# Kernel optimization log

Measured on AMD Instinct MI355X. Metric: run time of the kernel, lower is better.

## Reference

```python
import jax, jax.numpy as jnp
import numpy as np
import math

DIM = 1024
THETA = 10000.0


def rope_cos_sin(seq_len, dim, dtype=jnp.float32):
    # freqs over pairs: 1/theta^(2i/dim), angles = t * freq
    inv = 1.0 / (THETA ** (jnp.arange(0, dim, 2, dtype=jnp.float32) / dim))  # [dim/2]
    t = jnp.arange(seq_len, dtype=jnp.float32)
    ang = jnp.outer(t, inv)  # [S, dim/2]
    return jnp.cos(ang).astype(dtype), jnp.sin(ang).astype(dtype)


def apply_rotary(x, cos, sin):
    # x: [B, S, D]; treat consecutive pairs as complex (xr + i*xi)
    B, S, D = x.shape
    xr = x[..., 0::2]  # [B, S, D/2]
    xi = x[..., 1::2]
    or_ = xr * cos - xi * sin
    oi_ = xr * sin + xi * cos
    # interleave back: (..., D/2, 2) -> (..., D)
    return jnp.stack([or_, oi_], axis=-1).reshape(B, S, D)


def setup_inputs() -> dict:
    key = jax.random.key(0)
    ks = jax.random.split(key, 5)
    B, S, D = 4, 2048, DIM
    x = jax.random.normal(ks[0], (B, S, D), dtype=jnp.float32)
    s = 1.0 / math.sqrt(D)
    wq = jax.random.normal(ks[1], (D, D), dtype=jnp.float32) * s
    wk = jax.random.normal(ks[2], (D, D), dtype=jnp.float32) * s
    wv = jax.random.normal(ks[3], (D, D), dtype=jnp.float32) * s
    wo = jax.random.normal(ks[4], (D, D), dtype=jnp.float32) * s
    return {"x": x, "wq": wq, "wk": wk, "wv": wv, "wo": wo}


def reference(x, wq, wk, wv, wo):
    B, S, D = x.shape
    xq = jnp.einsum('bsd,ed->bse', x, wq)  # Linear: x @ W^T
    xk = jnp.einsum('bsd,ed->bse', x, wk)
    xv = jnp.einsum('bsd,ed->bse', x, wv)
    cos, sin = rope_cos_sin(S, D, x.dtype)
    xq = apply_rotary(xq, cos, sin)
    xk = apply_rotary(xk, cos, sin)
    scores = jnp.einsum('bqd,bkd->bqk', xq, xk) / jnp.sqrt(jnp.asarray(D, x.dtype))
    attn = jax.nn.softmax(scores, axis=-1)  # no causal mask in original
    out = jnp.einsum('bqk,bkd->bqd', attn, xv)
    return jnp.einsum('bsd,ed->bse', out, wo)
```

## Files before the change

kernel.cpp:

```cpp
#include <hip/hip_runtime.h>
#include <math.h>

typedef __attribute__((ext_vector_type(8))) short short8;
typedef __attribute__((ext_vector_type(4))) float f32x4;
typedef unsigned short u16;

__device__ __forceinline__ float b2f(u16 u) {
    union { unsigned u; float f; } c; c.u = ((unsigned)u) << 16; return c.f;
}
__device__ __forceinline__ u16 f2b(float f) {
    unsigned u = __float_as_uint(f);
    u += 0x7fffu + ((u >> 16) & 1u);
    return (u16)(u >> 16);
}

__device__ __forceinline__ void gl_lds16(const u16* g, u16* l) {
    __builtin_amdgcn_global_load_lds(
        (const __attribute__((address_space(1))) void*)g,
        (__attribute__((address_space(3))) void*)l,
        16, 0, 0);
}

__device__ __forceinline__ void wgbar() {
    asm volatile("" ::: "memory");
    __builtin_amdgcn_s_barrier();
    asm volatile("" ::: "memory");
}

__global__ __launch_bounds__(256) void cvt_f32_bf16(const float* __restrict__ src,
                                                    u16* __restrict__ dst, int n) {
    const int i = (blockIdx.x * 256 + threadIdx.x) * 8;
    if (i >= n) return;
    const float4 a = *(const float4*)&src[i];
    const float4 b = *(const float4*)&src[i + 4];
    short8 o;
    o[0] = (short)f2b(a.x); o[1] = (short)f2b(a.y);
    o[2] = (short)f2b(a.z); o[3] = (short)f2b(a.w);
    o[4] = (short)f2b(b.x); o[5] = (short)f2b(b.y);
    o[6] = (short)f2b(b.z); o[7] = (short)f2b(b.w);
    *(short8*)&dst[i] = o;
}

__global__ __launch_bounds__(256) void cvt_weights(
    const float* __restrict__ w0, const float* __restrict__ w1,
    const float* __restrict__ w2, const float* __restrict__ w3,
    u16* __restrict__ dst) {
    const int z = blockIdx.z;
    const float* src = (z == 0) ? w0 : (z == 1) ? w1 : (z == 2) ? w2 : w3;
    const int i = (blockIdx.x * 256 + threadIdx.x) * 8;
    const float4 a = *(const float4*)&src[i];
    const float4 b = *(const float4*)&src[i + 4];
    short8 o;
    o[0] = (short)f2b(a.x); o[1] = (short)f2b(a.y);
    o[2] = (short)f2b(a.z); o[3] = (short)f2b(a.w);
    o[4] = (short)f2b(b.x); o[5] = (short)f2b(b.y);
    o[6] = (short)f2b(b.z); o[7] = (short)f2b(b.w);
    *(short8*)&dst[(long)z * 1024 * 1024 + i] = o;
}

template<typename OT>
__device__ __forceinline__ void gemm256_body(
    const u16* __restrict__ A, const u16* __restrict__ W, OT* __restrict__ C,
    int lda, int ldw, int ldc, int K, float scale)
{
    __shared__ u16 lsA[2][2][8192];
    __shared__ u16 lsB[2][2][8192];

    const int m0 = blockIdx.y * 256;
    const int n0 = blockIdx.x * 256;
    const int t = threadIdx.x;
    const int lane = t & 63;
    const int w = t >> 6;
    const int wm = (w & 1) * 128;
    const int wn = (w >> 1) * 64;
    const int fr = lane & 15;
    const int fq = lane >> 4;

    const int srow = t >> 2;
    const int scol = (t & 3) * 8;
    const u16* pA0 = A + (long)(m0 + srow) * lda + scol;
    const u16* pA1 = A + (long)(m0 + 128 + srow) * lda + scol;
    const u16* pW0 = W + (long)(n0 + srow) * ldw + scol;
    const u16* pW1 = W + (long)(n0 + 128 + srow) * ldw + scol;
    const int tld = t * 8;

    f32x4 acc[8][4];
#pragma unroll
    for (int i = 0; i < 8; ++i)
#pragma unroll
        for (int j = 0; j < 4; ++j)
            acc[i][j] = (f32x4){0.f, 0.f, 0.f, 0.f};

    const int aoff = (wm + fr) * 32 + fq * 8;
    const int boff = (wn + fr) * 32 + fq * 8;

#define STAGE256(buf, h, ko) do { \
    gl_lds16(pA0 + (ko), &lsA[buf][h][tld]); \
    gl_lds16(pA1 + (ko), &lsA[buf][h][4096 + tld]); \
    gl_lds16(pW0 + (ko), &lsB[buf][h][tld]); \
    gl_lds16(pW1 + (ko), &lsB[buf][h][4096 + tld]); \
} while (0)

    const int nt = K >> 6;
    STAGE256(0, 0, 0);
    STAGE256(0, 1, 32);
    asm volatile("s_waitcnt vmcnt(4)" ::: "memory");
    wgbar();

    for (int tt = 0; tt < nt; ++tt) {
        const int p = tt & 1;
        const int kn = (tt + 1) << 6;
#pragma unroll
        for (int h = 0; h < 2; ++h) {
            short8 af[8], bfr[4];
#pragma unroll
            for (int m = 0; m < 8; ++m)
                af[m] = *(const short8*)&lsA[p][h][aoff + m * 512];
#pragma unroll
            for (int n = 0; n < 4; ++n)
                bfr[n] = *(const short8*)&lsB[p][h][boff + n * 512];
            if (tt + 1 < nt) {
                STAGE256(p ^ 1, h, kn + h * 32);
                asm volatile("s_waitcnt vmcnt(4)" ::: "memory");
            } else {
                asm volatile("s_waitcnt vmcnt(0)" ::: "memory");
            }
            wgbar();
            __builtin_amdgcn_s_setprio(1);
#pragma unroll
            for (int m = 0; m < 8; ++m)
#pragma unroll
                for (int n = 0; n < 4; ++n)
                    acc[m][n] = __builtin_amdgcn_mfma_f32_16x16x32_bf16(
                        af[m], bfr[n], acc[m][n], 0, 0, 0);
            __builtin_amdgcn_s_setprio(0);
        }
    }
#undef STAGE256

#pragma unroll
    for (int m = 0; m < 8; ++m) {
        const int row0 = m0 + wm + m * 16 + fq * 4;
#pragma unroll
        for (int n = 0; n < 4; ++n) {
            const int col = n0 + wn + n * 16 + fr;
#pragma unroll
            for (int r = 0; r < 4; ++r) {
                const float val = acc[m][n][r] * scale;
                if (sizeof(OT) == 2) {
                    ((u16*)C)[(long)(row0 + r) * ldc + col] = f2b(val);
                } else {
                    ((float*)C)[(long)(row0 + r) * ldc + col] = val;
                }
            }
        }
    }
}

template<typename OT>
__global__ __launch_bounds__(512, 2) void gemm256_bt(
    const u16* __restrict__ A, const u16* __restrict__ W, OT* __restrict__ C,
    int lda, int ldw, int ldc, int K,
    long sA, long sW, long sC, float scale)
{
    const int z = blockIdx.z;
    gemm256_body<OT>(A + (long)z * sA, W + (long)z * sW, C + (long)z * sC,
                     lda, ldw, ldc, K, scale);
}

__global__ __launch_bounds__(512, 2) void gemm256_dual(
    const u16* __restrict__ A0, const u16* __restrict__ W0, u16* __restrict__ C0,
    int lda0, int ldw0, int ldc0, long sA0, long sW0, long sC0, float scale0,
    const u16* __restrict__ A1, const u16* __restrict__ W1, u16* __restrict__ C1,
    int lda1, int ldw1, int ldc1, long sA1, long sW1, long sC1, float scale1)
{
    const int z = blockIdx.z;
    const u16 *A, *W; u16 *C; int lda, ldw, ldc; float scl;
    if (z < 4) {
        A = A0 + (long)z * sA0; W = W0 + (long)z * sW0; C = C0 + (long)z * sC0;
        lda = lda0; ldw = ldw0; ldc = ldc0; scl = scale0;
    } else {
        if (blockIdx.y >= 4) return;
        const int b = z - 4;
        A = A1 + (long)b * sA1; W = W1 + (long)b * sW1; C = C1 + (long)b * sC1;
        lda = lda1; ldw = ldw1; ldc = ldc1; scl = scale1;
    }
    gemm256_body<u16>(A, W, C, lda, ldw, ldc, 1024, scl);
}

template<typename OT>
__device__ __forceinline__ void gemm_body(
    const u16* __restrict__ A, const u16* __restrict__ W, OT* __restrict__ C,
    int lda, int ldw, int ldc, int K, float scale)
{
    __shared__ u16 lsA[2][128 * 32];
    __shared__ u16 lsB[2][128 * 32];

    const int m0 = blockIdx.y * 128;
    const int n0 = blockIdx.x * 128;
    const int t = threadIdx.x;
    const int lane = t & 63;
    const int wave = t >> 6;
    const int wm = (wave & 1) * 64;
    const int wn = (wave >> 1) * 64;

    const int sr = t >> 2;
    const int scol = ((t & 3) ^ ((t >> 3) & 3)) * 8;

    const u16* pa0 = A + (long)(m0 + sr) * lda + scol;
    const u16* pa1 = pa0 + (long)64 * lda;
    const u16* pw0 = W + (long)(n0 + sr) * ldw + scol;
    const u16* pw1 = pw0 + (long)64 * ldw;

    f32x4 acc[4][4];
#pragma unroll
    for (int i = 0; i < 4; ++i)
#pragma unroll
        for (int j = 0; j < 4; ++j)
            acc[i][j] = (f32x4){0.f, 0.f, 0.f, 0.f};

    const int fr = lane & 15;
    const int fq = lane >> 4;
    const int swz = (fq ^ ((fr >> 1) & 3)) * 8;
    const int aoff = (wm + fr) * 32 + swz;
    const int boff = (wn + fr) * 32 + swz;

    gl_lds16(pa0, &lsA[0][t * 8]);        pa0 += 32;
    gl_lds16(pa1, &lsA[0][2048 + t * 8]); pa1 += 32;
    gl_lds16(pw0, &lsB[0][t * 8]);        pw0 += 32;
    gl_lds16(pw1, &lsB[0][2048 + t * 8]); pw1 += 32;

    const int nsteps = K >> 5;
    int par = 0;
    for (int s = 0; s < nsteps; ++s) {
        __syncthreads();
        if (s + 1 < nsteps) {
            const int np = par ^ 1;
            gl_lds16(pa0, &lsA[np][t * 8]);        pa0 += 32;
            gl_lds16(pa1, &lsA[np][2048 + t * 8]); pa1 += 32;
            gl_lds16(pw0, &lsB[np][t * 8]);        pw0 += 32;
            gl_lds16(pw1, &lsB[np][2048 + t * 8]); pw1 += 32;
        }

        short8 af[4], bf[4];
#pragma unroll
        for (int i = 0; i < 4; ++i)
            af[i] = *(const short8*)&lsA[par][aoff + i * 512];
#pragma unroll
        for (int j = 0; j < 4; ++j)
            bf[j] = *(const short8*)&lsB[par][boff + j * 512];
#pragma unroll
        for (int i = 0; i < 4; ++i)
#pragma unroll
            for (int j = 0; j < 4; ++j)
                acc[i][j] = __builtin_amdgcn_mfma_f32_16x16x32_bf16(af[i], bf[j], acc[i][j], 0, 0, 0);
        par ^= 1;
    }

#pragma unroll
    for (int i = 0; i < 4; ++i) {
#pragma unroll
        for (int j = 0; j < 4; ++j) {
            const int row0 = m0 + wm + i * 16 + fq * 4;
            const int col = n0 + wn + j * 16 + fr;
#pragma unroll
            for (int r = 0; r < 4; ++r) {
                const int row = row0 + r;
                const float val = acc[i][j][r] * scale;
                if (sizeof(OT) == 2) {
                    ((u16*)C)[(long)row * ldc + col] = f2b(val);
                } else {
                    ((float*)C)[(long)row * ldc + col] = val;
                }
            }
        }
    }
}

template<typename OT>
__global__ __launch_bounds__(256) void gemm_bt(
    const u16* __restrict__ A, const u16* __restrict__ W, OT* __restrict__ C,
    int lda, int ldw, int ldc, int K,
    long sA, long sW, long sC, float scale)
{
    const int bz = blockIdx.z;
    gemm_body<OT>(A + (long)bz * sA, W + (long)bz * sW, C + (long)bz * sC,
                  lda, ldw, ldc, K, scale);
}

__global__ __launch_bounds__(256) void rope_kernel(u16* q, u16* k) {
    const int row = blockIdx.x;
    const int pos = row & 2047;
    u16* p = (blockIdx.y ? k : q) + (long)row * 1024;
#pragma unroll
    for (int it = 0; it < 2; ++it) {
        const int i = threadIdx.x + it * 256;
        const float e = (float)i * (1.0f / 512.0f);
        const float inv = powf(10000.0f, -e);
        const float ang = (float)pos * inv;
        float s, c;
        sincosf(ang, &s, &c);
        const float xr = b2f(p[2 * i]);
        const float xi = b2f(p[2 * i + 1]);
        p[2 * i]     = f2b(xr * c - xi * s);
        p[2 * i + 1] = f2b(xr * s + xi * c);
    }
}

__global__ __launch_bounds__(256) void softmax_kernel(const u16* __restrict__ S, u16* __restrict__ P) {
    const long row = blockIdx.x;
    const u16* src = S + row * 2048;
    u16* dst = P + row * 2048;
    const int t = threadIdx.x;
    const int lane = t & 63;
    const int wave = t >> 6;
    __shared__ float red[4];

    float v[8];
    const short8 raw = *(const short8*)&src[t * 8];
#pragma unroll
    for (int i = 0; i < 8; ++i) v[i] = b2f((u16)raw[i]);

    float m = v[0];
#pragma unroll
    for (int i = 1; i < 8; ++i) m = fmaxf(m, v[i]);
    for (int o = 32; o > 0; o >>= 1) m = fmaxf(m, __shfl_xor(m, o, 64));
    if (lane == 0) red[wave] = m;
    __syncthreads();
    m = fmaxf(fmaxf(red[0], red[1]), fmaxf(red[2], red[3]));
    __syncthreads();

    float sum = 0.f;
#pragma unroll
    for (int i = 0; i < 8; ++i) { v[i] = expf(v[i] - m); sum += v[i]; }
    for (int o = 32; o > 0; o >>= 1) sum += __shfl_xor(sum, o, 64);
    if (lane == 0) red[wave] = sum;
    __syncthreads();
    sum = red[0] + red[1] + red[2] + red[3];
    const float is = 1.0f / sum;

    short8 outv;
#pragma unroll
    for (int i = 0; i < 8; ++i) outv[i] = (short)f2b(v[i] * is);
    *(short8*)&dst[t * 8] = outv;
}

extern "C" void kernel_launch(void* const* d_in, const int* in_sizes, int n_in,
                              void* d_out, int out_size, void* d_ws, size_t ws_size,
                              hipStream_t stream)
{
    (void)in_sizes; (void)n_in; (void)out_size; (void)ws_size;
    const float* x  = (const float*)d_in[0];
    const float* wq = (const float*)d_in[1];
    const float* wk = (const float*)d_in[2];
    const float* wv = (const float*)d_in[3];
    const float* wo = (const float*)d_in[4];
    float* out = (float*)d_out;

    const long M1 = 1024 * 1024;
    u16* ws  = (u16*)d_ws;
    u16* xb  = ws;
    u16* wqb = xb + 8 * M1;
    u16* wob = wqb + 3 * M1;
    u16* q   = wqb + 4 * M1;
    u16* kk  = q + 8 * M1;
    u16* v   = kk + 8 * M1;
    u16* sc  = v + 8 * M1;
    u16* UT  = xb;

    const dim3 blk(256);
    const dim3 blk5(512);

    cvt_f32_bf16<<<dim3(4096), blk, 0, stream>>>(x, xb, 8 * 1024 * 1024);
    cvt_weights<<<dim3(512, 1, 4), blk, 0, stream>>>(wq, wk, wv, wo, wqb);

    gemm256_bt<u16><<<dim3(4, 32, 3), blk5, 0, stream>>>(xb, wqb, q,
        1024, 1024, 1024, 1024, 0, M1, 8 * M1, 1.0f);

    rope_kernel<<<dim3(8192, 2), blk, 0, stream>>>(q, kk);

    gemm256_dual<<<dim3(8, 8, 8), blk5, 0, stream>>>(
        q, kk, sc, 1024, 1024, 2048, 2 * M1, 2 * M1, 4 * M1, 0.03125f,
        wob, v, UT, 1024, 1024, 2048, 0, 2 * M1, 2 * M1, 1.0f);

    softmax_kernel<<<dim3(8192), blk, 0, stream>>>(sc, sc);

    gemm_bt<float><<<dim3(8, 16, 4), blk, 0, stream>>>(sc, UT, out,
        2048, 2048, 1024, 2048, 4 * M1, 2 * M1, 2 * M1, 1.0f);
}
```

Measured before the change: 326.3 us.

## Use four-slot LDS ring with deeper prefetch and XOR-swizzled LDS layout in GEMM

After: 323.1 us. About the same (-1.0%).

```diff
diff --git a/kernel.cpp b/kernel.cpp
--- a/kernel.cpp
+++ b/kernel.cpp
@@ -19,12 +19,6 @@
         (const __attribute__((address_space(1))) void*)g,
         (__attribute__((address_space(3))) void*)l,
         16, 0, 0);
-}
-
-__device__ __forceinline__ void wgbar() {
-    asm volatile("" ::: "memory");
-    __builtin_amdgcn_s_barrier();
-    asm volatile("" ::: "memory");
 }
 
 __global__ __launch_bounds__(256) void cvt_f32_bf16(const float* __restrict__ src,
@@ -63,8 +57,8 @@
     const u16* __restrict__ A, const u16* __restrict__ W, OT* __restrict__ C,
     int lda, int ldw, int ldc, int K, float scale)
 {
-    __shared__ u16 lsA[2][2][8192];
-    __shared__ u16 lsB[2][2][8192];
+    __shared__ u16 lsA[4 * 8192];
+    __shared__ u16 lsB[4 * 8192];
 
     const int m0 = blockIdx.y * 256;
     const int n0 = blockIdx.x * 256;
@@ -77,7 +71,7 @@
     const int fq = lane >> 4;
 
     const int srow = t >> 2;
-    const int scol = (t & 3) * 8;
+    const int scol = ((t & 3) ^ ((t >> 3) & 3)) * 8;
     const u16* pA0 = A + (long)(m0 + srow) * lda + scol;
     const u16* pA1 = A + (long)(m0 + 128 + srow) * lda + scol;
     const u16* pW0 = W + (long)(n0 + srow) * ldw + scol;
@@ -91,50 +85,57 @@
         for (int j = 0; j < 4; ++j)
             acc[i][j] = (f32x4){0.f, 0.f, 0.f, 0.f};
 
-    const int aoff = (wm + fr) * 32 + fq * 8;
-    const int boff = (wn + fr) * 32 + fq * 8;
-
-#define STAGE256(buf, h, ko) do { \
-    gl_lds16(pA0 + (ko), &lsA[buf][h][tld]); \
-    gl_lds16(pA1 + (ko), &lsA[buf][h][4096 + tld]); \
-    gl_lds16(pW0 + (ko), &lsB[buf][h][tld]); \
-    gl_lds16(pW1 + (ko), &lsB[buf][h][4096 + tld]); \
+    const int swz = (fq ^ ((fr >> 1) & 3)) * 8;
+    const int aoff = (wm + fr) * 32 + swz;
+    const int boff = (wn + fr) * 32 + swz;
+
+#define STAGE256(s) do { \
+    const int _sl = ((s) & 3) * 8192; const int _ko = (s) * 32; \
+    gl_lds16(pA0 + _ko, &lsA[_sl + tld]); \
+    gl_lds16(pA1 + _ko, &lsA[_sl + 4096 + tld]); \
+    gl_lds16(pW0 + _ko, &lsB[_sl + tld]); \
+    gl_lds16(pW1 + _ko, &lsB[_sl + 4096 + tld]); \
 } while (0)
 
-    const int nt = K >> 6;
-    STAGE256(0, 0, 0);
-    STAGE256(0, 1, 32);
-    asm volatile("s_waitcnt vmcnt(4)" ::: "memory");
-    wgbar();
-
-    for (int tt = 0; tt < nt; ++tt) {
-        const int p = tt & 1;
-        const int kn = (tt + 1) << 6;
-#pragma unroll
-        for (int h = 0; h < 2; ++h) {
-            short8 af[8], bfr[4];
-#pragma unroll
-            for (int m = 0; m < 8; ++m)
-                af[m] = *(const short8*)&lsA[p][h][aoff + m * 512];
+    const int n2 = K >> 5;
+
+    STAGE256(0);
+    STAGE256(1);
+    STAGE256(2);
+    asm volatile("s_waitcnt vmcnt(8)" ::: "memory");
+    __builtin_amdgcn_s_barrier();
+    __builtin_amdgcn_sched_barrier(0);
+
+    for (int st = 0; st < n2; ++st) {
+        const int slot = (st & 3) * 8192;
+        short8 af[8], bfr[4];
+#pragma unroll
+        for (int m = 0; m < 8; ++m)
+            af[m] = *(const short8*)&lsA[slot + aoff + m * 512];
+#pragma unroll
+        for (int n = 0; n < 4; ++n)
+            bfr[n] = *(const short8*)&lsB[slot + boff + n * 512];
+
+        if (st + 3 < n2) {
+            STAGE256(st + 3);
+            asm volatile("s_waitcnt vmcnt(8)" ::: "memory");
+        } else if (st + 2 < n2) {
+            asm volatile("s_waitcnt vmcnt(4)" ::: "memory");
+        } else if (st + 1 < n2) {
+            asm volatile("s_waitcnt vmcnt(0)" ::: "memory");
+        }
+        asm volatile("s_waitcnt lgkmcnt(0)" ::: "memory");
+        __builtin_amdgcn_s_barrier();
+        __builtin_amdgcn_sched_barrier(0);
+
+        __builtin_amdgcn_s_setprio(1);
+#pragma unroll
+        for (int m = 0; m < 8; ++m)
 #pragma unroll
             for (int n = 0; n < 4; ++n)
-                bfr[n] = *(const short8*)&lsB[p][h][boff + n * 512];
-            if (tt + 1 < nt) {
-                STAGE256(p ^ 1, h, kn + h * 32);
-                asm volatile("s_waitcnt vmcnt(4)" ::: "memory");
-            } else {
-                asm volatile("s_waitcnt vmcnt(0)" ::: "memory");
-            }
-            wgbar();
-            __builtin_amdgcn_s_setprio(1);
-#pragma unroll
-            for (int m = 0; m < 8; ++m)
-#pragma unroll
-                for (int n = 0; n < 4; ++n)
-                    acc[m][n] = __builtin_amdgcn_mfma_f32_16x16x32_bf16(
-                        af[m], bfr[n], acc[m][n], 0, 0, 0);
-            __builtin_amdgcn_s_setprio(0);
-        }
+                acc[m][n] = __builtin_amdgcn_mfma_f32_16x16x32_bf16(
+                    af[m], bfr[n], acc[m][n], 0, 0, 0);
+        __builtin_amdgcn_s_setprio(0);
     }
 #undef STAGE256
 
```
